# Optimization experiments

Hardware: AMD Instinct MI355X
Metric: run time of the kernel (lower is better)

The kernel has to match this reference:

```python
import jax, jax.numpy as jnp
import numpy as np
from jax import lax

B, CIN, H, W = 8, 256, 64, 64
CC = 128          # corr_channels
COUT = 64         # out_channels
KH = KW = 5       # corr_kernel_size
SH = SW = 1       # corr_stride
PT, PB = KH // 2, (KH + 1) // 2 - 1   # pad='k'
PL, PR = KW // 2, (KW + 1) // 2 - 1


def setup_inputs() -> dict:
    key = jax.random.key(0)
    k1, k2, k3, k4, k5 = jax.random.split(key, 5)
    x = jax.random.normal(k1, (B, CIN, H, W), dtype=jnp.float32)
    w_ext = jax.random.normal(k2, (CC, CIN, 3, 3), dtype=jnp.float32) * 0.02
    b_ext = jax.random.normal(k3, (CC,), dtype=jnp.float32) * 0.02
    w_reg = jax.random.normal(k4, (COUT, CC, KH, KW), dtype=jnp.float32) * 0.02
    b_reg = jax.random.normal(k5, (COUT,), dtype=jnp.float32) * 0.02
    return {"x": x, "w_ext": w_ext, "b_ext": b_ext, "w_reg": w_reg, "b_reg": b_reg}


def _forward(x, w_ext, b_ext, w_reg, b_reg):
    # feature extraction: 3x3 conv, padding 1
    f = lax.conv_general_dilated(x, w_ext, (1, 1), ((1, 1), (1, 1)))
    f = f + b_ext[None, :, None, None]
    # local autocorrelation: multiply each window element by the window center, per channel
    fp = jnp.pad(f, ((0, 0), (0, 0), (PT, PB), (PL, PR)))
    nH = (fp.shape[2] - KH) // SH + 1
    nW = (fp.shape[3] - KW) // SW + 1
    center = fp[:, :, KH // 2:KH // 2 + nH * SH:SH, KW // 2:KW // 2 + nW * SW:SW]  # [B,CC,nH,nW]
    patches = jnp.stack(
        [fp[:, :, u:u + nH * SH:SH, v:v + nW * SW:SW] for u in range(KH) for v in range(KW)],
        axis=-1)  # [B,CC,nH,nW,KH*KW]
    corr = patches * center[..., None]  # [B,CC,nH,nW,KH*KW]
    out = jnp.einsum('bcijk,ock->bijo', corr, w_reg.reshape(COUT, CC, KH * KW))
    out = out + b_reg
    return out.transpose(0, 3, 1, 2)  # permute=True -> [B, COUT, nH, nW]


def reference(x, w_ext, b_ext, w_reg, b_reg):
    return _forward(x, w_ext, b_ext, w_reg, b_reg)
```

## Files before the change

### kernel.cpp

```cpp
#include <hip/hip_runtime.h>
#include <hip/hip_bf16.h>

#define B_    8
#define CIN_  256
#define CC_   128
#define COUT_ 64
#define HP_   68
#define HPX_  (HP_ * HP_)
#define XQW_  66
#define XQPX_ (XQW_ * XQW_)

typedef __attribute__((ext_vector_type(8))) short bh8;
typedef __attribute__((ext_vector_type(4))) float f4;

__device__ __forceinline__ ushort f2bf(float f) {
    uint u = __float_as_uint(f);
    return (ushort)((u + 0x7fffu + ((u >> 16) & 1u)) >> 16);
}
__device__ __forceinline__ float bf2f(ushort s) {
    return __uint_as_float(((uint)s) << 16);
}
__device__ __forceinline__ short f2bf_c(float f) {
    __hip_bfloat16 h = __float2bfloat16(f);
    short s;
    __builtin_memcpy(&s, &h, 2);
    return s;
}

__global__ __launch_bounds__(256) void prep_misc(const float* __restrict__ w_ext,
                                                 const float* __restrict__ w_reg,
                                                 short* __restrict__ wg,
                                                 short* __restrict__ wa,
                                                 ushort* __restrict__ fpad_t) {
    int e = blockIdx.x * 256 + threadIdx.x;
    if (e < 67584) {
        int seg = e & 15;
        int t = e >> 4;
        int b = t / 528, rp = t - b * 528;
        int i, j;
        if (rp < 136) { i = rp / 68; j = rp - (rp / 68) * 68; }
        else if (rp < 272) { int r = rp - 136; i = 66 + r / 68; j = r - (r / 68) * 68; }
        else { int r = rp - 272; i = 2 + (r >> 2); int c = r & 3; j = (c < 2) ? c : c + 64; }
        uint4 z; z.x = 0u; z.y = 0u; z.z = 0u; z.w = 0u;
        *(uint4*)&fpad_t[(((size_t)b * HPX_) + i * HP_ + j) * 128 + seg * 8] = z;
        return;
    }
    e -= 67584;
    if (e < 294912) {
        int ci = e & 31;
        int t  = e >> 5;
        int cc = t & 127;
        int t2 = t >> 7;
        int rs = t2 % 9, cb = t2 / 9;
        wg[e] = (short)f2bf(w_ext[(cc * CIN_ + cb * 32 + ci) * 9 + rs]);
        return;
    }
    e -= 294912;
    if (e < 204800) {
        int ci = e & 31;
        int o  = (e >> 5) & 63;
        int rest = e >> 11;
        int k = rest % 25, q = rest / 25;
        wa[e] = (short)f2bf(w_reg[(o * CC_ + q * 32 + ci) * 25 + k]);
    }
}

__global__ __launch_bounds__(256) void prep_x(const float* __restrict__ x,
                                              ushort* __restrict__ xq) {
    __shared__ float xt[2][32][65];
    const int tid = threadIdx.x;
    const int rp = blockIdx.x, cb = blockIdx.y, b = blockIdx.z;

#pragma unroll
    for (int rr = 0; rr < 2; ++rr) {
        int y = rp * 2 + rr - 1;
        if ((unsigned)y < 64u) {
            int xx = tid & 63, wv = tid >> 6;
#pragma unroll
            for (int it = 0; it < 8; ++it) {
                int ci = it * 4 + wv;
                xt[rr][ci][xx] = x[(((size_t)(b * CIN_ + cb * 32 + ci)) * 64 + y) * 64 + xx];
            }
        }
    }
    __syncthreads();

    for (int e = tid; e < 528; e += 256) {
        int rr = e / 264, t = e - rr * 264;
        int hc = t >> 2, seg = t & 3;
        int y = rp * 2 + rr - 1, xx = hc - 1;
        uint pk[4] = {0u, 0u, 0u, 0u};
        if ((unsigned)y < 64u && (unsigned)xx < 64u) {
#pragma unroll
            for (int i = 0; i < 4; ++i) {
                uint lo = f2bf(xt[rr][seg * 8 + i * 2][xx]);
                uint hi = f2bf(xt[rr][seg * 8 + i * 2 + 1][xx]);
                pk[i] = lo | (hi << 16);
            }
        }
        uint4 v; v.x = pk[0]; v.y = pk[1]; v.z = pk[2]; v.w = pk[3];
        *(uint4*)&xq[((((size_t)(b * 8 + cb)) * XQPX_) + (rp * 2 + rr) * XQW_ + hc) * 32 + seg * 8] = v;
    }
}

__device__ __forceinline__ void stage_xq(const ushort* __restrict__ xq, short* __restrict__ dst,
                                         int b, int cb, int i0, int j0, int tid) {
    const ushort* base = xq + (((size_t)(b * 8 + cb)) * XQPX_) * 32;
    for (int e = tid; e < 400; e += 256) {
        int hp = e >> 2, seg = e & 3;
        int hr = hp / 10, hc = hp - hr * 10;
        const ushort* src = base + ((size_t)((i0 + hr) * XQW_ + (j0 + hc))) * 32 + seg * 8;
        *(bh8*)&dst[hp * 72 + seg * 8] = *(const bh8*)src;
    }
}

__global__ __launch_bounds__(256) void conv3x3_mfma(const ushort* __restrict__ xq,
                                                    const short* __restrict__ wg,
                                                    const float* __restrict__ bext,
                                                    ushort* __restrict__ fpad_t) {
    __shared__ __align__(16) short xh[2][100 * 72];
    const int tid = threadIdx.x;
    const int lane = tid & 63, wv = tid >> 6;
    const int j0 = blockIdx.x * 8, i0 = blockIdx.y * 8, b = blockIdx.z;
    const int l15 = lane & 15, kg = lane >> 4;
    const int cc0 = wv * 32;

    f4 acc[2][4] = {};

    stage_xq(xq, xh[0], b, 0, i0, j0, tid);
    __syncthreads();

    for (int cb = 0; cb < 8; ++cb) {
        const int buf = cb & 1;
        if (cb < 7) stage_xq(xq, xh[buf ^ 1], b, cb + 1, i0, j0, tid);

        const short* wbase = wg + (size_t)(cb * 9) * 128 * 32;
#pragma unroll
        for (int rs = 0; rs < 9; ++rs) {
            const int r = rs / 3, s = rs % 3;
            bh8 a[2], bb[4];
#pragma unroll
            for (int mm = 0; mm < 2; ++mm)
                a[mm] = *(const bh8*)(wbase + (rs * 128 + cc0 + mm * 16 + l15) * 32 + kg * 8);
#pragma unroll
            for (int nn = 0; nn < 4; ++nn) {
                int px = nn * 16 + l15, pi = px >> 3, pj = px & 7;
                int hidx = (pi + r) * 10 + (pj + s);
                bb[nn] = *(const bh8*)&xh[buf][hidx * 72 + kg * 8];
            }
#pragma unroll
            for (int mm = 0; mm < 2; ++mm)
#pragma unroll
                for (int nn = 0; nn < 4; ++nn)
                    acc[mm][nn] = __builtin_amdgcn_mfma_f32_16x16x32_bf16(
                        a[mm], bb[nn], acc[mm][nn], 0, 0, 0);
        }
        __syncthreads();
    }

#pragma unroll
    for (int mm = 0; mm < 2; ++mm) {
        const int ccb = cc0 + mm * 16 + kg * 4;
        float bv0 = bext[ccb + 0], bv1 = bext[ccb + 1];
        float bv2 = bext[ccb + 2], bv3 = bext[ccb + 3];
#pragma unroll
        for (int nn = 0; nn < 4; ++nn) {
            int px = nn * 16 + l15, pi = px >> 3, pj = px & 7;
            size_t row = (size_t)b * HPX_ + (2 + i0 + pi) * HP_ + (2 + j0 + pj);
            uint lo = (uint)f2bf(acc[mm][nn][0] + bv0) | ((uint)f2bf(acc[mm][nn][1] + bv1) << 16);
            uint hi = (uint)f2bf(acc[mm][nn][2] + bv2) | ((uint)f2bf(acc[mm][nn][3] + bv3) << 16);
            uint2 pk; pk.x = lo; pk.y = hi;
            *(uint2*)&fpad_t[row * 128 + ccb] = pk;
        }
    }
}

__global__ __launch_bounds__(256) void autocorr_mfma(const ushort* __restrict__ ft,
                                                     const short* __restrict__ wA,
                                                     const float* __restrict__ breg,
                                                     float* __restrict__ out) {
    __shared__ __align__(16) short flds[144 * 136];
    const int tid = threadIdx.x;
    const int lane = tid & 63, wv = tid >> 6;
    const int oh = wv >> 1, ph = wv & 1;
    const int j0 = blockIdx.x * 8, i0 = blockIdx.y * 8, b = blockIdx.z;
    const int l15 = lane & 15, kg = lane >> 4;

    for (int e = tid; e < 2304; e += 256) {
        int hp = e >> 4, seg = e & 15;
        int hr = hp / 12, hc = hp - hr * 12;
        const ushort* src = ft + ((size_t)b * HPX_ + (i0 + hr) * HP_ + (j0 + hc)) * 128 + seg * 8;
        *(bh8*)&flds[hp * 136 + seg * 8] = *(const bh8*)src;
    }
    __syncthreads();

    f4 acc[2][2] = {};
    int base_off[2], cen_off[2];
#pragma unroll
    for (int t = 0; t < 2; ++t) {
        int px = ph * 32 + t * 16 + l15;
        int pi = px >> 3, pj = px & 7;
        base_off[t] = (pi * 12 + pj) * 136 + kg * 8;
        cen_off[t]  = ((pi + 2) * 12 + (pj + 2)) * 136 + kg * 8;
    }

#pragma unroll 1
    for (int q = 0; q < 4; ++q) {
        float cen[2][8];
#pragma unroll
        for (int t = 0; t < 2; ++t) {
            bh8 c8 = *(const bh8*)&flds[cen_off[t] + q * 32];
#pragma unroll
            for (int jj = 0; jj < 8; ++jj) cen[t][jj] = bf2f((ushort)c8[jj]);
        }
        const short* wq = wA + q * (25 * 64 * 32);
#pragma unroll
        for (int k = 0; k < 25; ++k) {
            const int u = k / 5, v = k % 5;
            const int koff = (u * 12 + v) * 136;
            bh8 a[2];
#pragma unroll
            for (int mm = 0; mm < 2; ++mm)
                a[mm] = *(const bh8*)(wq + (k * 64 + oh * 32 + mm * 16 + l15) * 32 + kg * 8);
            bh8 bb[2];
#pragma unroll
            for (int t = 0; t < 2; ++t) {
                bh8 s8 = *(const bh8*)&flds[base_off[t] + q * 32 + koff];
#pragma unroll
                for (int jj = 0; jj < 8; ++jj) {
                    float p = bf2f((ushort)s8[jj]) * cen[t][jj];
                    bb[t][jj] = f2bf_c(p);
                }
            }
#pragma unroll
            for (int mm = 0; mm < 2; ++mm)
#pragma unroll
                for (int t = 0; t < 2; ++t)
                    acc[mm][t] = __builtin_amdgcn_mfma_f32_16x16x32_bf16(
                        a[mm], bb[t], acc[mm][t], 0, 0, 0);
        }
    }

#pragma unroll
    for (int mm = 0; mm < 2; ++mm) {
#pragma unroll
        for (int reg = 0; reg < 4; ++reg) {
            int o = oh * 32 + mm * 16 + kg * 4 + reg;
            float bv = breg[o];
#pragma unroll
            for (int t = 0; t < 2; ++t) {
                int px = ph * 32 + t * 16 + l15, pi = px >> 3, pj = px & 7;
                out[(((size_t)(b * COUT_ + o)) * 64 + i0 + pi) * 64 + j0 + pj] =
                    acc[mm][t][reg] + bv;
            }
        }
    }
}

extern "C" void kernel_launch(void* const* d_in, const int* in_sizes, int n_in,
                              void* d_out, int out_size, void* d_ws, size_t ws_size,
                              hipStream_t stream) {
    const float* x     = (const float*)d_in[0];
    const float* w_ext = (const float*)d_in[1];
    const float* b_ext = (const float*)d_in[2];
    const float* w_reg = (const float*)d_in[3];
    const float* b_reg = (const float*)d_in[4];
    float* out = (float*)d_out;

    char* ws = (char*)d_ws;
    const size_t FPADT_BYTES = (size_t)B_ * HPX_ * 128 * 2;
    const size_t WG_BYTES    = (size_t)8 * 9 * 128 * 32 * 2;
    const size_t WA_BYTES    = (size_t)4 * 25 * 64 * 32 * 2;
    ushort* fpad_t = (ushort*)ws;
    short*  wgq    = (short*)(ws + FPADT_BYTES);
    short*  wa     = (short*)(ws + FPADT_BYTES + WG_BYTES);
    ushort* xq     = (ushort*)(ws + FPADT_BYTES + WG_BYTES + WA_BYTES);

    const int PREP_TOTAL = 67584 + 294912 + 204800;
    prep_misc<<<(PREP_TOTAL + 255) / 256, 256, 0, stream>>>(w_ext, w_reg, wgq, wa, fpad_t);

    dim3 pgrid(33, 8, 8);
    prep_x<<<pgrid, 256, 0, stream>>>(x, xq);

    dim3 grid(8, 8, 8);
    conv3x3_mfma<<<grid, 256, 0, stream>>>(xq, wgq, b_ext, fpad_t);
    autocorr_mfma<<<grid, 256, 0, stream>>>(fpad_t, wa, b_reg, out);
}
```

Before: 82.71 us.

## Merge prep kernels into one launch and batch weight loads in MFMA loops

Fuses the two preparation kernels into a single launch that splits its blocks between weight/pad setup and input transposition, saving one kernel launch. In conv3x3 and autocorr it hoists all weight fragment loads for a channel block (or a kernel row) ahead of the MFMA loop so global loads can be issued together, and adds launch_bounds min-blocks hints of 2. The batched loads raise register pressure, which together with the occupancy hint may cause spills.

```diff
diff --git a/kernel.cpp b/kernel.cpp
--- a/kernel.cpp
+++ b/kernel.cpp
@@ -27,49 +27,53 @@
     return s;
 }
 
-__global__ __launch_bounds__(256) void prep_misc(const float* __restrict__ w_ext,
-                                                 const float* __restrict__ w_reg,
-                                                 short* __restrict__ wg,
-                                                 short* __restrict__ wa,
-                                                 ushort* __restrict__ fpad_t) {
-    int e = blockIdx.x * 256 + threadIdx.x;
-    if (e < 67584) {
-        int seg = e & 15;
-        int t = e >> 4;
-        int b = t / 528, rp = t - b * 528;
-        int i, j;
-        if (rp < 136) { i = rp / 68; j = rp - (rp / 68) * 68; }
-        else if (rp < 272) { int r = rp - 136; i = 66 + r / 68; j = r - (r / 68) * 68; }
-        else { int r = rp - 272; i = 2 + (r >> 2); int c = r & 3; j = (c < 2) ? c : c + 64; }
-        uint4 z; z.x = 0u; z.y = 0u; z.z = 0u; z.w = 0u;
-        *(uint4*)&fpad_t[(((size_t)b * HPX_) + i * HP_ + j) * 128 + seg * 8] = z;
-        return;
-    }
-    e -= 67584;
-    if (e < 294912) {
-        int ci = e & 31;
-        int t  = e >> 5;
-        int cc = t & 127;
-        int t2 = t >> 7;
-        int rs = t2 % 9, cb = t2 / 9;
-        wg[e] = (short)f2bf(w_ext[(cc * CIN_ + cb * 32 + ci) * 9 + rs]);
-        return;
-    }
-    e -= 294912;
-    if (e < 204800) {
-        int ci = e & 31;
-        int o  = (e >> 5) & 63;
-        int rest = e >> 11;
-        int k = rest % 25, q = rest / 25;
-        wa[e] = (short)f2bf(w_reg[(o * CC_ + q * 32 + ci) * 25 + k]);
-    }
-}
-
-__global__ __launch_bounds__(256) void prep_x(const float* __restrict__ x,
-                                              ushort* __restrict__ xq) {
+#define NB_MISC 2217
+__global__ __launch_bounds__(256) void prep_all(const float* __restrict__ x,
+                                                const float* __restrict__ w_ext,
+                                                const float* __restrict__ w_reg,
+                                                short* __restrict__ wg,
+                                                short* __restrict__ wa,
+                                                ushort* __restrict__ fpad_t,
+                                                ushort* __restrict__ xq) {
     __shared__ float xt[2][32][65];
     const int tid = threadIdx.x;
-    const int rp = blockIdx.x, cb = blockIdx.y, b = blockIdx.z;
+    if (blockIdx.x < NB_MISC) {
+        int e = blockIdx.x * 256 + tid;
+        if (e < 67584) {
+            int seg = e & 15;
+            int t = e >> 4;
+            int b = t / 528, rp = t - b * 528;
+            int i, j;
+            if (rp < 136) { i = rp / 68; j = rp - (rp / 68) * 68; }
+            else if (rp < 272) { int r = rp - 136; i = 66 + r / 68; j = r - (r / 68) * 68; }
+            else { int r = rp - 272; i = 2 + (r >> 2); int c = r & 3; j = (c < 2) ? c : c + 64; }
+            uint4 z; z.x = 0u; z.y = 0u; z.z = 0u; z.w = 0u;
+            *(uint4*)&fpad_t[(((size_t)b * HPX_) + i * HP_ + j) * 128 + seg * 8] = z;
+            return;
+        }
+        e -= 67584;
+        if (e < 294912) {
+            int ci = e & 31;
+            int t  = e >> 5;
+            int cc = t & 127;
+            int t2 = t >> 7;
+            int rs = t2 % 9, cb = t2 / 9;
+            wg[e] = (short)f2bf(w_ext[(cc * CIN_ + cb * 32 + ci) * 9 + rs]);
+            return;
+        }
+        e -= 294912;
+        if (e < 204800) {
+            int ci = e & 31;
+            int o  = (e >> 5) & 63;
+            int rest = e >> 11;
+            int k = rest % 25, q = rest / 25;
+            wa[e] = (short)f2bf(w_reg[(o * CC_ + q * 32 + ci) * 25 + k]);
+        }
+        return;
+    }
+
+    const int pid = blockIdx.x - NB_MISC;
+    const int rp = pid % 33, cb = (pid / 33) & 7, b = pid / 264;
 
 #pragma unroll
     for (int rr = 0; rr < 2; ++rr) {
@@ -114,10 +118,10 @@
     }
 }
 
-__global__ __launch_bounds__(256) void conv3x3_mfma(const ushort* __restrict__ xq,
-                                                    const short* __restrict__ wg,
-                                                    const float* __restrict__ bext,
-                                                    ushort* __restrict__ fpad_t) {
+__global__ __launch_bounds__(256, 2) void conv3x3_mfma(const ushort* __restrict__ xq,
+                                                       const short* __restrict__ wg,
+                                                       const float* __restrict__ bext,
+                                                       ushort* __restrict__ fpad_t) {
     __shared__ __align__(16) short xh[2][100 * 72];
     const int tid = threadIdx.x;
     const int lane = tid & 63, wv = tid >> 6;
@@ -135,13 +139,17 @@
         if (cb < 7) stage_xq(xq, xh[buf ^ 1], b, cb + 1, i0, j0, tid);
 
         const short* wbase = wg + (size_t)(cb * 9) * 128 * 32;
+        bh8 a[9][2];
+#pragma unroll
+        for (int rs = 0; rs < 9; ++rs)
+#pragma unroll
+            for (int mm = 0; mm < 2; ++mm)
+                a[rs][mm] = *(const bh8*)(wbase + (rs * 128 + cc0 + mm * 16 + l15) * 32 + kg * 8);
+
 #pragma unroll
         for (int rs = 0; rs < 9; ++rs) {
             const int r = rs / 3, s = rs % 3;
-            bh8 a[2], bb[4];
-#pragma unroll
-            for (int mm = 0; mm < 2; ++mm)
-                a[mm] = *(const bh8*)(wbase + (rs * 128 + cc0 + mm * 16 + l15) * 32 + kg * 8);
+            bh8 bb[4];
 #pragma unroll
             for (int nn = 0; nn < 4; ++nn) {
                 int px = nn * 16 + l15, pi = px >> 3, pj = px & 7;
@@ -153,7 +161,7 @@
 #pragma unroll
                 for (int nn = 0; nn < 4; ++nn)
                     acc[mm][nn] = __builtin_amdgcn_mfma_f32_16x16x32_bf16(
-                        a[mm], bb[nn], acc[mm][nn], 0, 0, 0);
+                        a[rs][mm], bb[nn], acc[mm][nn], 0, 0, 0);
         }
         __syncthreads();
     }
@@ -175,10 +183,10 @@
     }
 }
 
-__global__ __launch_bounds__(256) void autocorr_mfma(const ushort* __restrict__ ft,
-                                                     const short* __restrict__ wA,
-                                                     const float* __restrict__ breg,
-                                                     float* __restrict__ out) {
+__global__ __launch_bounds__(256, 2) void autocorr_mfma(const ushort* __restrict__ ft,
+                                                        const short* __restrict__ wA,
+                                                        const float* __restrict__ breg,
+                                                        float* __restrict__ out) {
     __shared__ __align__(16) short flds[144 * 136];
     const int tid = threadIdx.x;
     const int lane = tid & 63, wv = tid >> 6;
@@ -215,29 +223,34 @@
         }
         const short* wq = wA + q * (25 * 64 * 32);
 #pragma unroll
-        for (int k = 0; k < 25; ++k) {
-            const int u = k / 5, v = k % 5;
-            const int koff = (u * 12 + v) * 136;
-            bh8 a[2];
-#pragma unroll
-            for (int mm = 0; mm < 2; ++mm)
-                a[mm] = *(const bh8*)(wq + (k * 64 + oh * 32 + mm * 16 + l15) * 32 + kg * 8);
-            bh8 bb[2];
-#pragma unroll
-            for (int t = 0; t < 2; ++t) {
-                bh8 s8 = *(const bh8*)&flds[base_off[t] + q * 32 + koff];
-#pragma unroll
-                for (int jj = 0; jj < 8; ++jj) {
-                    float p = bf2f((ushort)s8[jj]) * cen[t][jj];
-                    bb[t][jj] = f2bf_c(p);
+        for (int u = 0; u < 5; ++u) {
+            bh8 a[5][2];
+#pragma unroll
+            for (int v = 0; v < 5; ++v)
+#pragma unroll
+                for (int mm = 0; mm < 2; ++mm)
+                    a[v][mm] = *(const bh8*)(wq + ((u * 5 + v) * 64 + oh * 32 + mm * 16 + l15) * 32 + kg * 8);
+
+#pragma unroll
+            for (int v = 0; v < 5; ++v) {
+                const int koff = (u * 12 + v) * 136;
+                bh8 bb[2];
+#pragma unroll
+                for (int t = 0; t < 2; ++t) {
+                    bh8 s8 = *(const bh8*)&flds[base_off[t] + q * 32 + koff];
+#pragma unroll
+                    for (int jj = 0; jj < 8; ++jj) {
+                        float p = bf2f((ushort)s8[jj]) * cen[t][jj];
+                        bb[t][jj] = f2bf_c(p);
+                    }
                 }
-            }
-#pragma unroll
-            for (int mm = 0; mm < 2; ++mm)
-#pragma unroll
-                for (int t = 0; t < 2; ++t)
-                    acc[mm][t] = __builtin_amdgcn_mfma_f32_16x16x32_bf16(
-                        a[mm], bb[t], acc[mm][t], 0, 0, 0);
+#pragma unroll
+                for (int mm = 0; mm < 2; ++mm)
+#pragma unroll
+                    for (int t = 0; t < 2; ++t)
+                        acc[mm][t] = __builtin_amdgcn_mfma_f32_16x16x32_bf16(
+                            a[v][mm], bb[t], acc[mm][t], 0, 0, 0);
+            }
         }
     }
 
@@ -276,11 +289,7 @@
     short*  wa     = (short*)(ws + FPADT_BYTES + WG_BYTES);
     ushort* xq     = (ushort*)(ws + FPADT_BYTES + WG_BYTES + WA_BYTES);
 
-    const int PREP_TOTAL = 67584 + 294912 + 204800;
-    prep_misc<<<(PREP_TOTAL + 255) / 256, 256, 0, stream>>>(w_ext, w_reg, wgq, wa, fpad_t);
-
-    dim3 pgrid(33, 8, 8);
-    prep_x<<<pgrid, 256, 0, stream>>>(x, xq);
+    prep_all<<<NB_MISC + 33 * 8 * 8, 256, 0, stream>>>(x, w_ext, w_reg, wgq, wa, fpad_t, xq);
 
     dim3 grid(8, 8, 8);
     conv3x3_mfma<<<grid, 256, 0, stream>>>(xq, wgq, b_ext, fpad_t);
```

Measured after the change: 93.56 us. +13.1%, slower.
